# Kernel tuning notes

Hardware: AMD Instinct MI355X
Metric: run time of the kernel (lower is better)

The kernel has to match this reference:

```python
import jax, jax.numpy as jnp
import numpy as np

B, N, D = 4, 4096, 1024

def setup_inputs() -> dict:
    key = jax.random.key(0)
    k1, k2 = jax.random.split(key)
    gates = jax.random.uniform(k1, (B, N, D), dtype=jnp.float32)
    inputs = jax.random.normal(k2, (B, N, D), dtype=jnp.float32)
    return {"gates": gates, "inputs": inputs}

def _binary_operator(a, b):
    # h = g * h_prev + x composed associatively:
    # (a_i, kv_i) o (a_j, kv_j) = (a_j * a_i, kv_j + a_j * kv_i)
    a_i, kv_i = a
    a_j, kv_j = b
    return (a_j * a_i, kv_j + a_j * kv_i)

def reference(gates, inputs):
    # AssocScan(use_accelerated=False, reverse=False), prev=None:
    # out[:, t] = gates[:, t] * out[:, t-1] + inputs[:, t]
    _, out = jax.lax.associative_scan(_binary_operator, (gates, inputs), axis=1)
    return out
```

## Files before the change

### kernel.cpp

```cpp
#include <hip/hip_runtime.h>


namespace {
constexpr int kB = 4;
constexpr int kN = 4096;
constexpr int kD = 1024;
constexpr int kChunks = 128;
constexpr int kT = kN / kChunks;
constexpr int kD4 = kD / 4;
constexpr int kAgg = kB * kChunks * kD4;
}

__global__ __launch_bounds__(256) void assoc_scan_phase1(
    const float4* __restrict__ g, const float4* __restrict__ x,
    float4* __restrict__ Ag, float4* __restrict__ Kv) {
  const int gid = blockIdx.x * 256 + threadIdx.x;
  const int d4 = gid & (kD4 - 1);
  const int c  = (gid >> 8) & (kChunks - 1);
  const int b  = gid >> 15;
  int idx = (b * kN + c * kT) * kD4 + d4;

  float4 a  = make_float4(1.f, 1.f, 1.f, 1.f);
  float4 kv = make_float4(0.f, 0.f, 0.f, 0.f);
#pragma unroll 4
  for (int i = 0; i < kT; ++i, idx += kD4) {
    const float4 gv = g[idx];
    const float4 xv = x[idx];
    a.x *= gv.x; a.y *= gv.y; a.z *= gv.z; a.w *= gv.w;
    kv.x = fmaf(gv.x, kv.x, xv.x);
    kv.y = fmaf(gv.y, kv.y, xv.y);
    kv.z = fmaf(gv.z, kv.z, xv.z);
    kv.w = fmaf(gv.w, kv.w, xv.w);
  }
  Ag[gid] = a;
  Kv[gid] = kv;
}

__global__ __launch_bounds__(256) void assoc_scan_phase2(
    const float4* __restrict__ Ag, const float4* __restrict__ Kv,
    float4* __restrict__ carry) {
  const int gid = blockIdx.x * 256 + threadIdx.x;
  const int d4 = gid & (kD4 - 1);
  const int b  = gid >> 8;

  float4 h = make_float4(0.f, 0.f, 0.f, 0.f);
  for (int c = 0; c < kChunks; ++c) {
    const int idx = (b * kChunks + c) * kD4 + d4;
    carry[idx] = h;
    const float4 a  = Ag[idx];
    const float4 kv = Kv[idx];
    h.x = fmaf(a.x, h.x, kv.x);
    h.y = fmaf(a.y, h.y, kv.y);
    h.z = fmaf(a.z, h.z, kv.z);
    h.w = fmaf(a.w, h.w, kv.w);
  }
}

__global__ __launch_bounds__(256) void assoc_scan_phase3(
    const float4* __restrict__ g, const float4* __restrict__ x,
    const float4* __restrict__ carry, float4* __restrict__ out) {
  const int gid = blockIdx.x * 256 + threadIdx.x;
  const int d4 = gid & (kD4 - 1);
  const int c  = (gid >> 8) & (kChunks - 1);
  const int b  = gid >> 15;
  int idx = (b * kN + c * kT) * kD4 + d4;

  float4 h = carry[gid];
#pragma unroll 4
  for (int i = 0; i < kT; ++i, idx += kD4) {
    const float4 gv = g[idx];
    const float4 xv = x[idx];
    h.x = fmaf(gv.x, h.x, xv.x);
    h.y = fmaf(gv.y, h.y, xv.y);
    h.z = fmaf(gv.z, h.z, xv.z);
    h.w = fmaf(gv.w, h.w, xv.w);
    out[idx] = h;
  }
}

extern "C" void kernel_launch(void* const* d_in, const int* in_sizes, int n_in,
                              void* d_out, int out_size, void* d_ws, size_t ws_size,
                              hipStream_t stream) {
  const float4* g = (const float4*)d_in[0];
  const float4* x = (const float4*)d_in[1];
  float4* out = (float4*)d_out;

  float4* Ag    = (float4*)d_ws;
  float4* Kv    = Ag + kAgg;
  float4* carry = Kv + kAgg;

  assoc_scan_phase1<<<kAgg / 256, 256, 0, stream>>>(g, x, Ag, Kv);
  assoc_scan_phase2<<<(kB * kD4) / 256, 256, 0, stream>>>(Ag, Kv, carry);
  assoc_scan_phase3<<<kAgg / 256, 256, 0, stream>>>(g, x, carry, out);
}
```

Measured before the change: 213.6 us.

## Parallelize chunk-carry scan across wavefront lanes and use more chunks

Raises the chunk count from 128 to 512 so phases 1 and 3 launch four times as many threads with shorter serial loops. Phase 2 changes from one thread walking all chunks serially to one 64-lane wavefront per column, which does a local scan over 8 chunks per lane and then a shuffle-based Hillis-Steele scan. The carry buffer now reuses the Ag workspace in place. In exchange, the aggregate traffic is four times larger, and it depends on the wavefront being 64 lanes wide.

```diff
diff --git a/kernel.cpp b/kernel.cpp
--- a/kernel.cpp
+++ b/kernel.cpp
@@ -5,10 +5,20 @@
 constexpr int kB = 4;
 constexpr int kN = 4096;
 constexpr int kD = 1024;
-constexpr int kChunks = 128;
+constexpr int kChunks = 512;
 constexpr int kT = kN / kChunks;
 constexpr int kD4 = kD / 4;
 constexpr int kAgg = kB * kChunks * kD4;
+constexpr int kCPL = kChunks / 64;
+}
+
+__device__ __forceinline__ float4 shfl_up4(float4 v, int off) {
+  float4 r;
+  r.x = __shfl_up(v.x, off);
+  r.y = __shfl_up(v.y, off);
+  r.z = __shfl_up(v.z, off);
+  r.w = __shfl_up(v.w, off);
+  return r;
 }
 
 __global__ __launch_bounds__(256) void assoc_scan_phase1(
@@ -17,12 +27,12 @@
   const int gid = blockIdx.x * 256 + threadIdx.x;
   const int d4 = gid & (kD4 - 1);
   const int c  = (gid >> 8) & (kChunks - 1);
-  const int b  = gid >> 15;
+  const int b  = gid >> 17;
   int idx = (b * kN + c * kT) * kD4 + d4;
 
   float4 a  = make_float4(1.f, 1.f, 1.f, 1.f);
   float4 kv = make_float4(0.f, 0.f, 0.f, 0.f);
-#pragma unroll 4
+#pragma unroll
   for (int i = 0; i < kT; ++i, idx += kD4) {
     const float4 gv = g[idx];
     const float4 xv = x[idx];
@@ -39,20 +49,54 @@
 __global__ __launch_bounds__(256) void assoc_scan_phase2(
     const float4* __restrict__ Ag, const float4* __restrict__ Kv,
     float4* __restrict__ carry) {
-  const int gid = blockIdx.x * 256 + threadIdx.x;
-  const int d4 = gid & (kD4 - 1);
-  const int b  = gid >> 8;
+  const int lane = threadIdx.x & 63;
+  const int col  = blockIdx.x * 4 + (threadIdx.x >> 6);
+  const int d4 = col & (kD4 - 1);
+  const int b  = col >> 8;
+  const int cBase = lane * kCPL;
 
-  float4 h = make_float4(0.f, 0.f, 0.f, 0.f);
-  for (int c = 0; c < kChunks; ++c) {
-    const int idx = (b * kChunks + c) * kD4 + d4;
-    carry[idx] = h;
-    const float4 a  = Ag[idx];
-    const float4 kv = Kv[idx];
-    h.x = fmaf(a.x, h.x, kv.x);
-    h.y = fmaf(a.y, h.y, kv.y);
-    h.z = fmaf(a.z, h.z, kv.z);
-    h.w = fmaf(a.w, h.w, kv.w);
+  float4 la[kCPL], lk[kCPL];
+  float4 ra = make_float4(1.f, 1.f, 1.f, 1.f);
+  float4 rk = make_float4(0.f, 0.f, 0.f, 0.f);
+#pragma unroll
+  for (int i = 0; i < kCPL; ++i) {
+    const int idx = (b * kChunks + cBase + i) * kD4 + d4;
+    la[i] = ra; lk[i] = rk;
+    const float4 a = Ag[idx];
+    const float4 k = Kv[idx];
+    rk.x = fmaf(a.x, rk.x, k.x);
+    rk.y = fmaf(a.y, rk.y, k.y);
+    rk.z = fmaf(a.z, rk.z, k.z);
+    rk.w = fmaf(a.w, rk.w, k.w);
+    ra.x *= a.x; ra.y *= a.y; ra.z *= a.z; ra.w *= a.w;
+  }
+
+#pragma unroll
+  for (int off = 1; off < 64; off <<= 1) {
+    const float4 pa = shfl_up4(ra, off);
+    const float4 pk = shfl_up4(rk, off);
+    if (lane >= off) {
+      rk.x = fmaf(ra.x, pk.x, rk.x);
+      rk.y = fmaf(ra.y, pk.y, rk.y);
+      rk.z = fmaf(ra.z, pk.z, rk.z);
+      rk.w = fmaf(ra.w, pk.w, rk.w);
+      ra.x *= pa.x; ra.y *= pa.y; ra.z *= pa.z; ra.w *= pa.w;
+    }
+  }
+  float4 ek = shfl_up4(rk, 1);
+  if (lane == 0) {
+    ek = make_float4(0.f, 0.f, 0.f, 0.f);
+  }
+
+#pragma unroll
+  for (int i = 0; i < kCPL; ++i) {
+    const int idx = (b * kChunks + cBase + i) * kD4 + d4;
+    float4 ck;
+    ck.x = fmaf(la[i].x, ek.x, lk[i].x);
+    ck.y = fmaf(la[i].y, ek.y, lk[i].y);
+    ck.z = fmaf(la[i].z, ek.z, lk[i].z);
+    ck.w = fmaf(la[i].w, ek.w, lk[i].w);
+    carry[idx] = ck;
   }
 }
 
@@ -62,11 +106,11 @@
   const int gid = blockIdx.x * 256 + threadIdx.x;
   const int d4 = gid & (kD4 - 1);
   const int c  = (gid >> 8) & (kChunks - 1);
-  const int b  = gid >> 15;
+  const int b  = gid >> 17;
   int idx = (b * kN + c * kT) * kD4 + d4;
 
   float4 h = carry[gid];
-#pragma unroll 4
+#pragma unroll
   for (int i = 0; i < kT; ++i, idx += kD4) {
     const float4 gv = g[idx];
     const float4 xv = x[idx];
@@ -87,9 +131,9 @@
 
   float4* Ag    = (float4*)d_ws;
   float4* Kv    = Ag + kAgg;
-  float4* carry = Kv + kAgg;
+  float4* carry = Ag;
 
   assoc_scan_phase1<<<kAgg / 256, 256, 0, stream>>>(g, x, Ag, Kv);
-  assoc_scan_phase2<<<(kB * kD4) / 256, 256, 0, stream>>>(Ag, Kv, carry);
+  assoc_scan_phase2<<<(kB * kD4) / 4, 256, 0, stream>>>(Ag, Kv, carry);
   assoc_scan_phase3<<<kAgg / 256, 256, 0, stream>>>(g, x, carry, out);
 }
```

New measurement: 200.4 us. -6.2%, faster.
